# Kernel tuning notes

Hardware: AMD Instinct MI355X
Metric: run time of the kernel (lower is better)

Reference implementation:

```python
import jax, jax.numpy as jnp
import numpy as np

N_NODES = 50000
N_EDGES = 800000
IN_F = 128
OUT_F = 64


def setup_inputs() -> dict:
    key = jax.random.key(0)
    k1, k2, k3, k4, k5 = jax.random.split(key, 5)
    x = jax.random.normal(k1, (N_NODES, IN_F), dtype=jnp.float32)
    edge_index = jax.random.randint(k2, (2, N_EDGES), 0, N_NODES, dtype=jnp.int64)
    edge_weight = jax.random.uniform(k3, (N_EDGES,), dtype=jnp.float32)
    # Linear(in,out,bias=False): store as [in, out] so h = x @ W
    W = jax.random.normal(k4, (IN_F, OUT_F), dtype=jnp.float32) * (1.0 / np.sqrt(IN_F))
    # Linear(2*out, 1, bias=False): store as [2*out] vector
    a = jax.random.normal(k5, (2 * OUT_F,), dtype=jnp.float32) * (1.0 / np.sqrt(2 * OUT_F))
    return {"x": x, "edge_index": edge_index, "edge_weight": edge_weight, "W": W, "a": a}


def reference(x, edge_index, edge_weight, W, a):
    N = x.shape[0]
    F = W.shape[1]
    src, dst = edge_index[0], edge_index[1]
    h = x @ W  # [N, F]
    # a([h_src ; h_dst]) == h_src @ a[:F] + h_dst @ a[F:]  (no edge-level concat)
    s_src = h @ a[:F]   # [N]
    s_dst = h @ a[F:]   # [N]
    e = s_src[src] + s_dst[dst]            # [E]
    alpha = jax.nn.leaky_relu(e, negative_slope=0.2) * edge_weight
    alpha = alpha - jnp.max(alpha)         # global max subtraction, as in source
    alpha_exp = jnp.exp(alpha)             # [E]
    alpha_sum = jax.ops.segment_sum(alpha_exp, dst, num_segments=N)  # [N]
    alpha_norm = alpha_exp / (alpha_sum[dst] + 1e-8)                 # [E] (dropout = identity, eval mode)
    out = jax.ops.segment_sum(h[src] * alpha_norm[:, None], dst, num_segments=N)  # [N, F]
    return jax.nn.elu(out)
```

## Files before the change

### kernel.cpp

```cpp
#include <hip/hip_runtime.h>
#include <hip/hip_bf16.h>
#include <math.h>

#define FIN 128
#define FOUT 64
#define TM 64
#define XS_STRIDE 136

#define DB 64
#define CAP 1280
#define NBMAX 1024
#define TILE_A 2048
#define EPT_A 8

typedef __attribute__((ext_vector_type(8))) short short8;
typedef __attribute__((ext_vector_type(4))) float floatx4;

static __device__ __forceinline__ unsigned short f2bf(float f) {
  __hip_bfloat16 b = __float2bfloat16(f);
  return *reinterpret_cast<unsigned short*>(&b);
}

__global__ __launch_bounds__(256) void k_prep(
    const float* __restrict__ W, const float* __restrict__ a,
    unsigned short* __restrict__ Wt, float* __restrict__ Wa,
    int* __restrict__ bcur, int nbuck)
{
  int t = threadIdx.x, b = blockIdx.x;
  int gid = b * 256 + t;
  int stride = gridDim.x * 256;
  for (int i = gid; i < nbuck; i += stride) bcur[i] = 0;
  for (int i = gid; i < FIN * FOUT; i += stride) {
    int f = i >> 7, k = i & 127;
    Wt[i] = f2bf(W[k * FOUT + f]);
  }
  if (b == 0) {
    int which = t >> 7, k = t & 127;
    const float* av = a + which * FOUT;
    const float* wr = W + k * FOUT;
    float c = 0.f;
#pragma unroll
    for (int f = 0; f < FOUT; f++) c = fmaf(wr[f], av[f], c);
    Wa[which * FIN + k] = c;
  }
}

__global__ __launch_bounds__(256) void k_gemm(
    const float* __restrict__ x, const unsigned short* __restrict__ Wt,
    const float* __restrict__ Wa, unsigned short* __restrict__ hbf,
    float* __restrict__ s_src, float* __restrict__ s_dst, int N)
{
  __shared__ unsigned short xsb[TM][XS_STRIDE];
  __shared__ float wa[2][FIN];
  int t = threadIdx.x;
  int n0 = blockIdx.x * TM;

  wa[t >> 7][t & 127] = Wa[t];

#pragma unroll
  for (int i = 0; i < 8; i++) {
    int idx = t + i * 256;
    int row = idx >> 5, c4 = (idx & 31) * 4;
    int n = n0 + row;
    float4 v = make_float4(0.f, 0.f, 0.f, 0.f);
    if (n < N) v = *(const float4*)&x[(size_t)n * FIN + c4];
    ushort4 u = make_ushort4(f2bf(v.x), f2bf(v.y), f2bf(v.z), f2bf(v.w));
    *(ushort4*)&xsb[row][c4] = u;
  }
  __syncthreads();

  {
    int row = t >> 2, which = (t >> 1) & 1, half = t & 1;
    int n = n0 + row;
    float c = 0.f;
    if (n < N) {
      const float4* xr = (const float4*)&x[(size_t)n * FIN + half * 64];
      const float* wv = &wa[which][half * 64];
#pragma unroll
      for (int kk = 0; kk < 16; kk++) {
        float4 xv = xr[kk];
        c = fmaf(xv.x, wv[kk * 4 + 0],
            fmaf(xv.y, wv[kk * 4 + 1],
            fmaf(xv.z, wv[kk * 4 + 2],
            fmaf(xv.w, wv[kk * 4 + 3], c))));
      }
    }
    c += __shfl_xor(c, 1);
    if (half == 0 && n < N) {
      if (which == 0) s_src[n] = c; else s_dst[n] = c;
    }
  }

  int lane = t & 63, w = t >> 6;
  int m = lane & 15, q = lane >> 4;

  short8 bf[4][4];
#pragma unroll
  for (int k0 = 0; k0 < 4; k0++)
#pragma unroll
    for (int j = 0; j < 4; j++)
      bf[k0][j] = *(const short8*)(Wt + (j * 16 + m) * FIN + k0 * 32 + q * 8);

  floatx4 acc[4];
#pragma unroll
  for (int j = 0; j < 4; j++) acc[j] = (floatx4){0.f, 0.f, 0.f, 0.f};

#pragma unroll
  for (int k0 = 0; k0 < 4; k0++) {
    short8 af = *(const short8*)&xsb[w * 16 + m][k0 * 32 + q * 8];
#pragma unroll
    for (int j = 0; j < 4; j++)
      acc[j] = __builtin_amdgcn_mfma_f32_16x16x32_bf16(af, bf[k0][j], acc[j], 0, 0, 0);
  }

#pragma unroll
  for (int j = 0; j < 4; j++)
#pragma unroll
    for (int r = 0; r < 4; r++) {
      int n = n0 + w * 16 + q * 4 + r;
      if (n < N) hbf[(size_t)n * FOUT + j * 16 + m] = f2bf(acc[j][r]);
    }
}

__global__ __launch_bounds__(256) void k_bucketA(
    const int* __restrict__ src, const int* __restrict__ dst,
    const float* __restrict__ ew, const float* __restrict__ s_src,
    const float* __restrict__ s_dst, int* __restrict__ bcur,
    uint2* __restrict__ inter, int E, int nbuck)
{
  __shared__ uint2 stage[TILE_A];
  __shared__ int hist[NBMAX];
  __shared__ int sbase[NBMAX];
  __shared__ int gbase[NBMAX];
  __shared__ int wsum[4];

  int t = threadIdx.x;
  int base = blockIdx.x * TILE_A;
  int cntTile = E - base; if (cntTile > TILE_A) cntTile = TILE_A;

  for (int i = t; i < nbuck; i += 256) hist[i] = 0;
  __syncthreads();

  unsigned key[EPT_A]; float aev[EPT_A]; int lpos[EPT_A];
#pragma unroll
  for (int i = 0; i < EPT_A; i++) {
    int e = base + t + i * 256;
    lpos[i] = -1;
    if (e < E) {
      int s = src[e], d = dst[e];
      float v = s_src[s] + s_dst[d];
      v = (v > 0.f) ? v : 0.2f * v;
      v *= ew[e];
      key[i] = ((unsigned)d << 16) | (unsigned)s;
      aev[i] = expf(v);
      lpos[i] = atomicAdd(&hist[d >> 6], 1);
    }
  }
  __syncthreads();

  int i0 = t * 4;
  int c0 = (i0 + 0 < nbuck) ? hist[i0 + 0] : 0;
  int c1 = (i0 + 1 < nbuck) ? hist[i0 + 1] : 0;
  int c2 = (i0 + 2 < nbuck) ? hist[i0 + 2] : 0;
  int c3 = (i0 + 3 < nbuck) ? hist[i0 + 3] : 0;
  int ts = c0 + c1 + c2 + c3;
  int lane = t & 63, wid = t >> 6;
  int inc = ts;
#pragma unroll
  for (int o = 1; o < 64; o <<= 1) {
    int up = __shfl_up(inc, o);
    if (lane >= o) inc += up;
  }
  if (lane == 63) wsum[wid] = inc;
  __syncthreads();
  int woff = 0;
  for (int w = 0; w < wid; w++) woff += wsum[w];
  int run = woff + inc - ts;
  if (i0 + 0 < nbuck) sbase[i0 + 0] = run; run += c0;
  if (i0 + 1 < nbuck) sbase[i0 + 1] = run; run += c1;
  if (i0 + 2 < nbuck) sbase[i0 + 2] = run; run += c2;
  if (i0 + 3 < nbuck) sbase[i0 + 3] = run;
  __syncthreads();

  for (int b = t; b < nbuck; b += 256)
    if (hist[b] > 0) gbase[b] = atomicAdd(&bcur[b], hist[b]);
  __syncthreads();

#pragma unroll
  for (int i = 0; i < EPT_A; i++)
    if (lpos[i] >= 0) {
      int b = key[i] >> 22;
      stage[sbase[b] + lpos[i]] = make_uint2(key[i], __float_as_uint(aev[i]));
    }
  __syncthreads();

  for (int i = t; i < cntTile; i += 256) {
    uint2 en = stage[i];
    int b = en.x >> 22;
    int slot = gbase[b] + (i - sbase[b]);
    if (slot < CAP) inter[(size_t)b * CAP + slot] = en;
  }
}

__global__ __launch_bounds__(512) void k_bucketB(
    const uint2* __restrict__ inter, const int* __restrict__ bcur,
    const unsigned short* __restrict__ hbf, float* __restrict__ out, int N)
{
  __shared__ uint2 ss[CAP];
  __shared__ int hist[DB];
  __shared__ int rp[DB];
  int b = blockIdx.x;
  int t = threadIdx.x;
  int cnt = bcur[b]; if (cnt > CAP) cnt = CAP;

  if (t < DB) hist[t] = 0;
  __syncthreads();

  const uint2* bin = inter + (size_t)b * CAP;
  unsigned kx[3], ka[3]; int lp[3], dl[3];
#pragma unroll
  for (int i = 0; i < 3; i++) {
    int p = t + i * 512;
    lp[i] = -1;
    if (p < cnt) {
      uint2 en = bin[p];
      kx[i] = en.x; ka[i] = en.y;
      dl[i] = (en.x >> 16) & (DB - 1);
      lp[i] = atomicAdd(&hist[dl[i]], 1);
    }
  }
  __syncthreads();

  if (t < DB) {
    int v = hist[t];
    int inc = v;
#pragma unroll
    for (int o = 1; o < 64; o <<= 1) {
      int up = __shfl_up(inc, o);
      if (t >= o) inc += up;
    }
    rp[t] = inc - v;
  }
  __syncthreads();

#pragma unroll
  for (int i = 0; i < 3; i++)
    if (lp[i] >= 0) ss[rp[dl[i]] + lp[i]] = make_uint2(kx[i], ka[i]);
  __syncthreads();

  int grp = t >> 3, l = t & 7;
  int n = b * DB + grp;
  int beg = rp[grp];
  int end = beg + hist[grp];

  float acc[8];
#pragma unroll
  for (int i = 0; i < 8; i++) acc[i] = 0.f;
  float asum = 0.f;

  for (int p = beg; p < end; p += 2) {
    uint2 e0 = ss[p];
    float ae0 = __uint_as_float(e0.y);
    uint4 r0 = ((const uint4*)(hbf + ((size_t)(e0.x & 0xFFFFu) << 6)))[l];
    float ae1 = 0.f;
    uint4 r1 = make_uint4(0u, 0u, 0u, 0u);
    if (p + 1 < end) {
      uint2 e1 = ss[p + 1];
      ae1 = __uint_as_float(e1.y);
      r1 = ((const uint4*)(hbf + ((size_t)(e1.x & 0xFFFFu) << 6)))[l];
    }
    asum += ae0 + ae1;
    const unsigned* u0 = (const unsigned*)&r0;
    const unsigned* u1 = (const unsigned*)&r1;
#pragma unroll
    for (int i = 0; i < 4; i++) {
      float2 f0 = __bfloat1622float2(*(const __hip_bfloat162*)&u0[i]);
      float2 f1 = __bfloat1622float2(*(const __hip_bfloat162*)&u1[i]);
      acc[2 * i]     = fmaf(ae0, f0.x, acc[2 * i]);
      acc[2 * i + 1] = fmaf(ae0, f0.y, acc[2 * i + 1]);
      acc[2 * i]     = fmaf(ae1, f1.x, acc[2 * i]);
      acc[2 * i + 1] = fmaf(ae1, f1.y, acc[2 * i + 1]);
    }
  }

  if (n < N) {
    float inv = 1.f / (asum + 1e-8f);
    float v[8];
#pragma unroll
    for (int i = 0; i < 8; i++) {
      v[i] = acc[i] * inv;
      v[i] = (v[i] > 0.f) ? v[i] : expm1f(v[i]);
    }
    float* op = &out[(size_t)n * FOUT + l * 8];
    *(float4*)op       = make_float4(v[0], v[1], v[2], v[3]);
    *(float4*)(op + 4) = make_float4(v[4], v[5], v[6], v[7]);
  }
}

extern "C" void kernel_launch(void* const* d_in, const int* in_sizes, int n_in,
                              void* d_out, int out_size, void* d_ws, size_t ws_size,
                              hipStream_t stream)
{
  const float* x  = (const float*)d_in[0];
  const int*   ei = (const int*)d_in[1];
  const float* ew = (const float*)d_in[2];
  const float* W  = (const float*)d_in[3];
  const float* a  = (const float*)d_in[4];
  float* out = (float*)d_out;

  const int N = in_sizes[0] / FIN;
  const int E = in_sizes[2];
  const int* src = ei;
  const int* dst = ei + E;
  const int nbuck = (N + DB - 1) / DB;

  unsigned short* Wt = (unsigned short*)d_ws;
  float* Wa    = (float*)(Wt + FIN * FOUT);
  unsigned short* hbf = (unsigned short*)(Wa + 256);
  float* ssrc  = (float*)(hbf + (size_t)N * FOUT);
  float* sdst  = ssrc + N;
  int*   bcur  = (int*)(sdst + N);
  uint2* inter = (uint2*)(bcur + 800);

  k_prep<<<33, 256, 0, stream>>>(W, a, Wt, Wa, bcur, nbuck);
  k_gemm<<<(N + TM - 1) / TM, 256, 0, stream>>>(x, Wt, Wa, hbf, ssrc, sdst, N);
  k_bucketA<<<(E + TILE_A - 1) / TILE_A, 256, 0, stream>>>(src, dst, ew, ssrc, sdst, bcur, inter, E, nbuck);
  k_bucketB<<<nbuck, 512, 0, stream>>>(inter, bcur, hbf, out, N);
}
```

Measured before the change: 136.4 us.

## Fold prep kernel into GEMM and derive attention scores from MFMA accumulators

Removes the separate prep kernel. Each GEMM block now converts W to bf16 into shared memory itself, zeroes the bucket counters, and computes s_src/s_dst from the MFMA accumulators with a shuffle reduction instead of a separate fp32 dot-product pass over x. The bucketing kernel also switches to the fast __expf and doubles its tile size to 4096 edges per block. The costs are redundant W loading and conversion in every block, bf16-rounded inputs for the scores, and more LDS use and register pressure in bucketA.

```diff
diff --git a/kernel.cpp b/kernel.cpp
--- a/kernel.cpp
+++ b/kernel.cpp
@@ -10,8 +10,8 @@
 #define DB 64
 #define CAP 1280
 #define NBMAX 1024
-#define TILE_A 2048
-#define EPT_A 8
+#define TILE_A 4096
+#define EPT_A 16
 
 typedef __attribute__((ext_vector_type(8))) short short8;
 typedef __attribute__((ext_vector_type(4))) float floatx4;
@@ -21,41 +21,24 @@
   return *reinterpret_cast<unsigned short*>(&b);
 }
 
-__global__ __launch_bounds__(256) void k_prep(
-    const float* __restrict__ W, const float* __restrict__ a,
-    unsigned short* __restrict__ Wt, float* __restrict__ Wa,
-    int* __restrict__ bcur, int nbuck)
-{
-  int t = threadIdx.x, b = blockIdx.x;
-  int gid = b * 256 + t;
-  int stride = gridDim.x * 256;
-  for (int i = gid; i < nbuck; i += stride) bcur[i] = 0;
-  for (int i = gid; i < FIN * FOUT; i += stride) {
-    int f = i >> 7, k = i & 127;
-    Wt[i] = f2bf(W[k * FOUT + f]);
-  }
-  if (b == 0) {
-    int which = t >> 7, k = t & 127;
-    const float* av = a + which * FOUT;
-    const float* wr = W + k * FOUT;
-    float c = 0.f;
-#pragma unroll
-    for (int f = 0; f < FOUT; f++) c = fmaf(wr[f], av[f], c);
-    Wa[which * FIN + k] = c;
-  }
-}
-
 __global__ __launch_bounds__(256) void k_gemm(
-    const float* __restrict__ x, const unsigned short* __restrict__ Wt,
-    const float* __restrict__ Wa, unsigned short* __restrict__ hbf,
-    float* __restrict__ s_src, float* __restrict__ s_dst, int N)
+    const float* __restrict__ x, const float* __restrict__ W,
+    const float* __restrict__ a, unsigned short* __restrict__ hbf,
+    float* __restrict__ s_src, float* __restrict__ s_dst,
+    int* __restrict__ bcur, int N)
 {
   __shared__ unsigned short xsb[TM][XS_STRIDE];
-  __shared__ float wa[2][FIN];
+  __shared__ unsigned short Wl[FOUT][XS_STRIDE];
   int t = threadIdx.x;
   int n0 = blockIdx.x * TM;
 
-  wa[t >> 7][t & 127] = Wa[t];
+  int gid = blockIdx.x * 256 + t;
+  if (gid < 800) bcur[gid] = 0;
+
+  for (int i = t; i < FIN * FOUT; i += 256) {
+    int k = i >> 6, f = i & 63;
+    Wl[f][k] = f2bf(W[i]);
+  }
 
 #pragma unroll
   for (int i = 0; i < 8; i++) {
@@ -69,28 +52,6 @@
   }
   __syncthreads();
 
-  {
-    int row = t >> 2, which = (t >> 1) & 1, half = t & 1;
-    int n = n0 + row;
-    float c = 0.f;
-    if (n < N) {
-      const float4* xr = (const float4*)&x[(size_t)n * FIN + half * 64];
-      const float* wv = &wa[which][half * 64];
-#pragma unroll
-      for (int kk = 0; kk < 16; kk++) {
-        float4 xv = xr[kk];
-        c = fmaf(xv.x, wv[kk * 4 + 0],
-            fmaf(xv.y, wv[kk * 4 + 1],
-            fmaf(xv.z, wv[kk * 4 + 2],
-            fmaf(xv.w, wv[kk * 4 + 3], c))));
-      }
-    }
-    c += __shfl_xor(c, 1);
-    if (half == 0 && n < N) {
-      if (which == 0) s_src[n] = c; else s_dst[n] = c;
-    }
-  }
-
   int lane = t & 63, w = t >> 6;
   int m = lane & 15, q = lane >> 4;
 
@@ -99,7 +60,7 @@
   for (int k0 = 0; k0 < 4; k0++)
 #pragma unroll
     for (int j = 0; j < 4; j++)
-      bf[k0][j] = *(const short8*)(Wt + (j * 16 + m) * FIN + k0 * 32 + q * 8);
+      bf[k0][j] = *(const short8*)&Wl[j * 16 + m][k0 * 32 + q * 8];
 
   floatx4 acc[4];
 #pragma unroll
@@ -111,6 +72,32 @@
 #pragma unroll
     for (int j = 0; j < 4; j++)
       acc[j] = __builtin_amdgcn_mfma_f32_16x16x32_bf16(af, bf[k0][j], acc[j], 0, 0, 0);
+  }
+
+  float av1[4], av2[4];
+#pragma unroll
+  for (int j = 0; j < 4; j++) {
+    av1[j] = a[j * 16 + m];
+    av2[j] = a[FOUT + j * 16 + m];
+  }
+  float s1r[4], s2r[4];
+#pragma unroll
+  for (int r = 0; r < 4; r++) {
+    float c1 = 0.f, c2 = 0.f;
+#pragma unroll
+    for (int j = 0; j < 4; j++) {
+      c1 = fmaf(acc[j][r], av1[j], c1);
+      c2 = fmaf(acc[j][r], av2[j], c2);
+    }
+    s1r[r] = c1; s2r[r] = c2;
+  }
+#pragma unroll
+  for (int o = 1; o < 16; o <<= 1) {
+#pragma unroll
+    for (int r = 0; r < 4; r++) {
+      s1r[r] += __shfl_xor(s1r[r], o);
+      s2r[r] += __shfl_xor(s2r[r], o);
+    }
   }
 
 #pragma unroll
@@ -120,6 +107,13 @@
       int n = n0 + w * 16 + q * 4 + r;
       if (n < N) hbf[(size_t)n * FOUT + j * 16 + m] = f2bf(acc[j][r]);
     }
+  if (m == 0) {
+#pragma unroll
+    for (int r = 0; r < 4; r++) {
+      int n = n0 + w * 16 + q * 4 + r;
+      if (n < N) { s_src[n] = s1r[r]; s_dst[n] = s2r[r]; }
+    }
+  }
 }
 
 __global__ __launch_bounds__(256) void k_bucketA(
@@ -152,7 +146,7 @@
       v = (v > 0.f) ? v : 0.2f * v;
       v *= ew[e];
       key[i] = ((unsigned)d << 16) | (unsigned)s;
-      aev[i] = expf(v);
+      aev[i] = __expf(v);
       lpos[i] = atomicAdd(&hist[d >> 6], 1);
     }
   }
@@ -314,16 +308,13 @@
   const int* dst = ei + E;
   const int nbuck = (N + DB - 1) / DB;
 
-  unsigned short* Wt = (unsigned short*)d_ws;
-  float* Wa    = (float*)(Wt + FIN * FOUT);
-  unsigned short* hbf = (unsigned short*)(Wa + 256);
+  unsigned short* hbf = (unsigned short*)d_ws;
   float* ssrc  = (float*)(hbf + (size_t)N * FOUT);
   float* sdst  = ssrc + N;
   int*   bcur  = (int*)(sdst + N);
   uint2* inter = (uint2*)(bcur + 800);
 
-  k_prep<<<33, 256, 0, stream>>>(W, a, Wt, Wa, bcur, nbuck);
-  k_gemm<<<(N + TM - 1) / TM, 256, 0, stream>>>(x, Wt, Wa, hbf, ssrc, sdst, N);
+  k_gemm<<<(N + TM - 1) / TM, 256, 0, stream>>>(x, W, a, hbf, ssrc, sdst, bcur, N);
   k_bucketA<<<(E + TILE_A - 1) / TILE_A, 256, 0, stream>>>(src, dst, ew, ssrc, sdst, bcur, inter, E, nbuck);
   k_bucketB<<<nbuck, 512, 0, stream>>>(inter, bcur, hbf, out, N);
 }
```

New measurement: 126.6 us. 7.2% less time.
